# Kernel tuning notes

Measured on AMD Instinct MI355X. Metric: run time of the kernel, lower is better.

Reference implementation:

```python
import jax, jax.numpy as jnp
import numpy as np

H = 256
EPS = 1e-5
RBF_GAMMA = 10.0
RBF_CENTERS = jnp.asarray(np.arange(0.0, np.pi, 0.1), dtype=jnp.float32)  # 32 centers


def layer_norm(x, g, b):
    m = x.mean(-1, keepdims=True)
    v = ((x - m) ** 2).mean(-1, keepdims=True)
    return (x - m) * jax.lax.rsqrt(v + EPS) * g + b


def gin(src, dst, n_nodes, node_feat, edge_feat, w1, b1, w2, b2):
    # message = h_src + h_edge ; sum-aggregate at dst ; 2-layer MLP
    msg = node_feat[src] + edge_feat                                  # [E, H]
    agg = jax.ops.segment_sum(msg, dst, num_segments=n_nodes)        # [N, H]
    return jax.nn.relu(agg @ w1 + b1) @ w2 + b2


def graph_normal(gid, n_graphs, x):
    # divide each node feature by sqrt(#nodes in its graph)
    cnt = jax.ops.segment_sum(jnp.ones((x.shape[0],), x.dtype), gid, num_segments=n_graphs)
    return x * jax.lax.rsqrt(jnp.maximum(cnt, 1.0))[gid][:, None]


def geognn_block(src, dst, gid, n_graphs, node_hidden, edge_feat, w1, b1, w2, b2, ln_g, ln_b):
    out = gin(src, dst, node_hidden.shape[0], node_hidden, edge_feat, w1, b1, w2, b2)
    out = layer_norm(out, ln_g, ln_b)
    out = graph_normal(gid, n_graphs, out)
    # activation=False, dropout is identity in eval mode
    return out + node_hidden


def setup_inputs() -> dict:
    key = jax.random.key(0)
    ks = jax.random.split(key, 24)
    N, E, A, G = 65536, 131072, 262144, 2048
    nC = RBF_CENTERS.shape[0]
    s = 1.0 / np.sqrt(H)
    inp = {
        "node_hidden": jax.random.normal(ks[0], (N, H), jnp.float32),
        "edge_hidden": jax.random.normal(ks[1], (E, H), jnp.float32),
        "bond_angle": jax.random.uniform(ks[2], (A,), jnp.float32) * np.float32(np.pi),
        "ab_src": jax.random.randint(ks[3], (N * 2,), 0, N).astype(jnp.int64)[:E],
        "ab_dst": jax.random.randint(ks[4], (E,), 0, N).astype(jnp.int64),
        "ba_src": jax.random.randint(ks[5], (A,), 0, E).astype(jnp.int64),
        "ba_dst": jax.random.randint(ks[6], (A,), 0, E).astype(jnp.int64),
        "node_gid": jnp.sort(jax.random.randint(ks[7], (N,), 0, G)).astype(jnp.int64),
        "bond_gid": jnp.sort(jax.random.randint(ks[8], (E,), 0, G)).astype(jnp.int64),
        "num_graphs": G,
        # bond-angle RBF linear
        "rbf_w": jax.random.normal(ks[9], (nC, H), jnp.float32) / np.sqrt(nC),
        "rbf_b": jnp.zeros((H,), jnp.float32),
        # bond_angle_gnn (GIN MLP + LayerNorm)
        "ba_w1": jax.random.normal(ks[10], (H, 2 * H), jnp.float32) * s,
        "ba_b1": jnp.zeros((2 * H,), jnp.float32),
        "ba_w2": jax.random.normal(ks[11], (2 * H, H), jnp.float32) * s,
        "ba_b2": jnp.zeros((H,), jnp.float32),
        "ba_ln_g": jnp.ones((H,), jnp.float32),
        "ba_ln_b": jnp.zeros((H,), jnp.float32),
        # atom_bond_gnn
        "ab_w1": jax.random.normal(ks[12], (H, 2 * H), jnp.float32) * s,
        "ab_b1": jnp.zeros((2 * H,), jnp.float32),
        "ab_w2": jax.random.normal(ks[13], (2 * H, H), jnp.float32) * s,
        "ab_b2": jnp.zeros((H,), jnp.float32),
        "ab_ln_g": jnp.ones((H,), jnp.float32),
        "ab_ln_b": jnp.zeros((H,), jnp.float32),
    }
    return inp


def reference(node_hidden, edge_hidden, bond_angle, ab_src, ab_dst, ba_src, ba_dst,
              node_gid, bond_gid, num_graphs, rbf_w, rbf_b,
              ba_w1, ba_b1, ba_w2, ba_b2, ba_ln_g, ba_ln_b,
              ab_w1, ab_b1, ab_w2, ab_b2, ab_ln_g, ab_ln_b):
    # RBF encode bond angles -> angle edge features [A, H]
    rbf = jnp.exp(-RBF_GAMMA * (bond_angle[:, None] - RBF_CENTERS[None, :]) ** 2)
    angle_hidden = rbf @ rbf_w + rbf_b
    # bond-angle GNN updates bond features (nodes of bond_angle graph)
    edge_out = geognn_block(ba_src, ba_dst, bond_gid, num_graphs,
                            edge_hidden, angle_hidden,
                            ba_w1, ba_b1, ba_w2, ba_b2, ba_ln_g, ba_ln_b)
    # atom-bond GNN updates atom features using updated bond features as edge feats
    node_out = geognn_block(ab_src, ab_dst, node_gid, num_graphs,
                            node_hidden, edge_out,
                            ab_w1, ab_b1, ab_w2, ab_b2, ab_ln_g, ab_ln_b)
    # average pooling over atoms per graph
    cnt = jax.ops.segment_sum(jnp.ones((node_out.shape[0],), node_out.dtype), node_gid,
                              num_segments=num_graphs)
    graph_repr = jax.ops.segment_sum(node_out, node_gid, num_segments=num_graphs) / jnp.maximum(cnt, 1.0)[:, None]
    return node_out, edge_out, graph_repr
```

## Files before the change

### kernel.cpp

```cpp
#include <hip/hip_runtime.h>

#define HDIM 256
#define LNEPS 1e-5f

typedef float f32x4 __attribute__((ext_vector_type(4)));
typedef short bf16x8 __attribute__((ext_vector_type(8)));

static __device__ __forceinline__ unsigned short f2b(float f) {
  union { float f; unsigned u; } v; v.f = f;
  return (unsigned short)((v.u + 0x7fffu + ((v.u >> 16) & 1u)) >> 16);
}
static __device__ __forceinline__ unsigned pk2(float lo, float hi) {
  return (unsigned)f2b(lo) | ((unsigned)f2b(hi) << 16);
}

__global__ void pack_all_kernel(const float* __restrict__ w1a, const float* __restrict__ w2a,
                                const float* __restrict__ w1b, const float* __restrict__ w2b,
                                unsigned short* __restrict__ o1a, unsigned short* __restrict__ o2a,
                                unsigned short* __restrict__ o1b, unsigned short* __restrict__ o2b) {
  int sel = blockIdx.x >> 9;
  int o = (blockIdx.x & 511) * 256 + threadIdx.x;
  if (sel == 0 || sel == 2) {
    const float* in = (sel == 0) ? w1a : w1b;
    unsigned short* out = (sel == 0) ? o1a : o1b;
    int ke = o & 7, n1l = (o >> 3) & 127, lg = (o >> 10) & 3, sl = o >> 12;
    int h = sl >> 3, kk = sl & 7;
    int k = kk * 32 + lg * 8 + ke, n1 = h * 128 + n1l;
    out[o] = f2b(in[k * 512 + n1]);
  } else {
    const float* in = (sel == 1) ? w2a : w2b;
    unsigned short* out = (sel == 1) ? o2a : o2b;
    int ke = o & 7, n2l = (o >> 3) & 127, lg = (o >> 10) & 3, sl = o >> 12;
    int h = sl >> 3, r = sl & 7, h2 = r >> 2, kk2 = r & 3;
    int k2 = h * 128 + kk2 * 32 + lg * 8 + ke, n2 = h2 * 128 + n2l;
    out[o] = f2b(in[k2 * 256 + n2]);
  }
}

__global__ void prep_kernel(const int* __restrict__ node_gid, const int* __restrict__ bond_gid,
                            const int* __restrict__ ab_dst, const int* __restrict__ ba_dst,
                            int* cnt_node, int* cnt_bond, int* deg_n, int* deg_e,
                            int N, int E, int A) {
  int i = blockIdx.x * 256 + threadIdx.x;
  if (i < N) atomicAdd(&cnt_node[node_gid[i]], 1);
  if (i < E) {
    atomicAdd(&cnt_bond[bond_gid[i]], 1);
    atomicAdd(&deg_n[ab_dst[i]], 1);
  }
  if (i < A) atomicAdd(&deg_e[ba_dst[i]], 1);
}

__global__ void scan1_both_kernel(const int* __restrict__ degE, const int* __restrict__ degN,
                                  int* __restrict__ offE, int* __restrict__ offN,
                                  int* __restrict__ bsum, int E, int N, int nbE) {
  int b = blockIdx.x;
  const int* deg; int* excl; int* bs; int n; int bb;
  if (b < nbE) { deg = degE; excl = offE; bs = bsum; n = E; bb = b; }
  else { deg = degN; excl = offN; bs = bsum + 512; n = N; bb = b - nbE; }
  int t = threadIdx.x;
  int i = bb * 256 + t;
  int v = (i < n) ? deg[i] : 0;
  int lane = t & 63, w = t >> 6;
  int s = v;
#pragma unroll
  for (int d = 1; d < 64; d <<= 1) {
    int u = __shfl_up(s, d);
    if (lane >= d) s += u;
  }
  __shared__ int wsum[4];
  if (lane == 63) wsum[w] = s;
  __syncthreads();
  int base = 0;
  for (int ww = 0; ww < w; ++ww) base += wsum[ww];
  if (i < n) excl[i] = base + s - v;
  if (t == 255) bs[bb] = base + s;
}

__global__ void scan2_both_kernel(int* __restrict__ bsum, int nbE, int nbN) {
  int* bs = bsum + blockIdx.x * 512;
  int nb = (blockIdx.x == 0) ? nbE : nbN;
  int t = threadIdx.x;
  int v = (t < nb) ? bs[t] : 0;
  int lane = t & 63, w = t >> 6;
  int s = v;
#pragma unroll
  for (int d = 1; d < 64; d <<= 1) {
    int u = __shfl_up(s, d);
    if (lane >= d) s += u;
  }
  __shared__ int wsum[16];
  if (lane == 63) wsum[w] = s;
  __syncthreads();
  int base = 0;
  for (int ww = 0; ww < w; ++ww) base += wsum[ww];
  if (t < nb) bs[t] = base + s - v;
}

__global__ void scan3f_kernel(int* __restrict__ offE, int* __restrict__ offN,
                              const int* __restrict__ bsum,
                              const int* __restrict__ cnt_node, const int* __restrict__ cnt_bond,
                              float* fac_node, float* fac_bond, float* recip_node,
                              int E, int N, int G, int nbE, int nbN) {
  int b = blockIdx.x;
  if (b < nbE) {
    int i = b * 256 + threadIdx.x;
    if (i < E) offE[i] += bsum[b];
  } else if (b < nbE + nbN) {
    int bb = b - nbE;
    int i = bb * 256 + threadIdx.x;
    if (i < N) offN[i] += bsum[512 + bb];
  } else {
    int g = (b - nbE - nbN) * 256 + threadIdx.x;
    if (g < G) {
      float cn = fmaxf((float)cnt_node[g], 1.f);
      float cb = fmaxf((float)cnt_bond[g], 1.f);
      fac_node[g] = rsqrtf(cn);
      fac_bond[g] = rsqrtf(cb);
      recip_node[g] = 1.f / cn;
    }
  }
}

__global__ void fill_both_kernel(const int* __restrict__ ba_dst, const int* __restrict__ ab_dst,
                                 const int* __restrict__ offE, const int* __restrict__ offN,
                                 int* __restrict__ curE, int* __restrict__ curN,
                                 int* __restrict__ csrE, int* __restrict__ csrN,
                                 int A, int E, int nbA) {
  int b = blockIdx.x;
  if (b < nbA) {
    int i = b * 256 + threadIdx.x;
    if (i < A) {
      int d = ba_dst[i];
      int p = atomicAdd(&curE[d], 1);
      csrE[offE[d] + p] = i;
    }
  } else {
    int i = (b - nbA) * 256 + threadIdx.x;
    if (i < E) {
      int d = ab_dst[i];
      int p = atomicAdd(&curN[d], 1);
      csrN[offN[d] + p] = i;
    }
  }
}

__global__ __launch_bounds__(256) void angle_gather_kernel(
    const float* __restrict__ bond_angle, const int* __restrict__ ba_src,
    const float* __restrict__ edge_hidden,
    const int* __restrict__ off, const int* __restrict__ deg, const int* __restrict__ csr,
    const float* __restrict__ rbf_w, const float* __restrict__ rbf_b,
    float* __restrict__ agg_e, int E) {
  __shared__ float rbfw_s[32 * 256];
  int t = threadIdx.x;
  int w = t >> 6, lane = t & 63;
#pragma unroll
  for (int i = 0; i < 8; ++i)
    *(f32x4*)&rbfw_s[(t + i * 256) * 4] = *(const f32x4*)&rbf_w[(t + i * 256) * 4];
  __syncthreads();
  int c4 = lane * 4;
  f32x4 bv = *(const f32x4*)&rbf_b[c4];
  float cc = 0.1f * (float)(lane & 31);
  for (int rr = 0; rr < 2; ++rr) {
    int d = blockIdx.x * 8 + w * 2 + rr;
    if (d >= E) break;
    int start = off[d], cnt = deg[d];
    f32x4 acc = (f32x4)0.f;
    float rbfs = 0.f;
    for (int base = 0; base < cnt; base += 64) {
      int n = cnt - base; if (n > 64) n = 64;
      float av = 0.f;
      int s = 0;
      if (lane < n) {
        int a = csr[start + base + lane];
        av = bond_angle[a];
        s = ba_src[a];
      }
#pragma unroll 4
      for (int i = 0; i < n; ++i) {
        float avi = __shfl(av, i);
        int si = __shfl(s, i);
        if (lane < 32) {
          float dd = avi - cc;
          rbfs += __expf(-10.f * dd * dd);
        }
        acc += *(const f32x4*)&edge_hidden[(size_t)si * HDIM + c4];
      }
    }
#pragma unroll 8
    for (int k = 0; k < 32; ++k) {
      float rv = __shfl(rbfs, k);
      f32x4 wv = *(const f32x4*)&rbfw_s[k * 256 + c4];
      acc[0] += rv * wv[0]; acc[1] += rv * wv[1];
      acc[2] += rv * wv[2]; acc[3] += rv * wv[3];
    }
    float fc = (float)cnt;
    acc[0] += fc * bv[0]; acc[1] += fc * bv[1];
    acc[2] += fc * bv[2]; acc[3] += fc * bv[3];
    *(f32x4*)&agg_e[(size_t)d * HDIM + c4] = acc;
  }
}

__global__ __launch_bounds__(256) void node_gather_kernel(
    const float* __restrict__ node_hidden, const float* __restrict__ edge_out,
    const int* __restrict__ ab_src,
    const int* __restrict__ off, const int* __restrict__ deg, const int* __restrict__ csr,
    float* __restrict__ agg_n, int N) {
  int w = threadIdx.x >> 6, lane = threadIdx.x & 63;
  int d = blockIdx.x * 4 + w;
  if (d >= N) return;
  int c4 = lane * 4;
  int start = off[d], cnt = deg[d];
  f32x4 acc = (f32x4)0.f;
  for (int base = 0; base < cnt; base += 64) {
    int n = cnt - base; if (n > 64) n = 64;
    int e = 0, s = 0;
    if (lane < n) {
      e = csr[start + base + lane];
      s = ab_src[e];
    }
#pragma unroll 4
    for (int i = 0; i < n; ++i) {
      int ei = __shfl(e, i);
      int si = __shfl(s, i);
      f32x4 a = *(const f32x4*)&edge_out[(size_t)ei * HDIM + c4];
      f32x4 b = *(const f32x4*)&node_hidden[(size_t)si * HDIM + c4];
      acc += a;
      acc += b;
    }
  }
  *(f32x4*)&agg_n[(size_t)d * HDIM + c4] = acc;
}

template <int POOL>
__global__ __launch_bounds__(256, 4) void mlp_kernel(
    const float* agg_in, float* out_rows,
    const float* __restrict__ residual, const int* __restrict__ gid,
    const float* __restrict__ gfactor,
    const unsigned short* __restrict__ w1p, const float* __restrict__ b1,
    const unsigned short* __restrict__ w2p, const float* __restrict__ b2,
    const float* __restrict__ ln_g, const float* __restrict__ ln_b,
    float* pool_out, int M) {
  __shared__ __align__(16) char smem[40960];
  char* Xb = smem;
  char* Hb = smem + 16384;
  char* Wb = smem + 24576;
  char* OutsB = smem;
  float* psA = (float*)(smem + 32768);
  float* psB = (float*)(smem + 33280);
  float* fstat = (float*)(smem + 33792);
  float* gfs = (float*)(smem + 34048);
  int* gid_s = (int*)(smem + 34176);

  int t = threadIdx.x;
  int row0 = blockIdx.x * 32;
  int w = t >> 6, lane = t & 63;
  int l15 = lane & 15, lg = lane >> 4;

  auto slab_ptr = [&](int ss) -> const uint4* {
    int hh = ss >> 4, r = ss & 15;
    const unsigned short* p = (r < 8) ? (w1p + (size_t)(hh * 8 + r) * 4096)
                                      : (w2p + (size_t)(hh * 8 + (r - 8)) * 4096);
    return (const uint4*)p;
  };

  uint4 rA0, rA1, rB0, rB1;

  {
    const uint4* g0 = slab_ptr(0);
    uint4 s0a = g0[t], s0b = g0[t + 256];
    const uint4* g1 = slab_ptr(1);
    rA0 = g1[t]; rA1 = g1[t + 256];
    int row = t >> 3;
    int c0 = (t & 7) * 32;
    int gr = row0 + row; if (gr >= M) gr = M - 1;
    const float* src = agg_in + (size_t)gr * HDIM + c0;
#pragma unroll
    for (int i = 0; i < 4; ++i) {
      f32x4 a = *(const f32x4*)(src + i * 8);
      f32x4 b = *(const f32x4*)(src + i * 8 + 4);
      int byte = (row * 512 + (c0 + i * 8) * 2) ^ ((row & 7) << 4);
      *(uint4*)(Xb + byte) =
          make_uint4(pk2(a[0], a[1]), pk2(a[2], a[3]), pk2(b[0], b[1]), pk2(b[2], b[3]));
    }
    *(uint4*)(Wb + t * 16) = s0a;
    *(uint4*)(Wb + (t + 256) * 16) = s0b;
  }
  __syncthreads();

  f32x4 acc2[2][4];
#pragma unroll
  for (int mt = 0; mt < 2; ++mt)
#pragma unroll
    for (int nf = 0; nf < 4; ++nf) acc2[mt][nf] = (f32x4)0.f;

  int s = 0;
  for (int h = 0; h < 4; ++h) {
    f32x4 acc1[2][2];
#pragma unroll
    for (int tt = 0; tt < 2; ++tt)
#pragma unroll
      for (int mt = 0; mt < 2; ++mt) acc1[tt][mt] = (f32x4)0.f;

    for (int kk = 0; kk < 8; ++kk) {
      if (s + 2 < 64) { const uint4* g = slab_ptr(s + 2); rB0 = g[t]; rB1 = g[t + 256]; }
      const char* buf = Wb + (s & 1) * 8192;
      bf16x8 xfr[2], afr[2];
#pragma unroll
      for (int mt = 0; mt < 2; ++mt) {
        int m = mt * 16 + l15;
        int byte = (m * 512 + kk * 64 + lg * 16) ^ ((m & 7) << 4);
        xfr[mt] = *(const bf16x8*)(Xb + byte);
      }
#pragma unroll
      for (int tt = 0; tt < 2; ++tt)
        afr[tt] = *(const bf16x8*)(buf + lg * 2048 + (w * 32 + tt * 16 + l15) * 16);
#pragma unroll
      for (int tt = 0; tt < 2; ++tt)
#pragma unroll
        for (int mt = 0; mt < 2; ++mt)
          acc1[tt][mt] = __builtin_amdgcn_mfma_f32_16x16x32_bf16(afr[tt], xfr[mt], acc1[tt][mt], 0, 0, 0);

      if (kk == 7) {
#pragma unroll
        for (int tt = 0; tt < 2; ++tt) {
          f32x4 b1v = *(const f32x4*)&b1[h * 128 + w * 32 + tt * 16 + lg * 4];
#pragma unroll
          for (int mt = 0; mt < 2; ++mt) {
            f32x4 v = acc1[tt][mt] + b1v;
            v[0] = fmaxf(v[0], 0.f); v[1] = fmaxf(v[1], 0.f);
            v[2] = fmaxf(v[2], 0.f); v[3] = fmaxf(v[3], 0.f);
            int m = mt * 16 + l15;
            int n1l = w * 32 + tt * 16 + lg * 4;
            int byte = (m * 256 + n1l * 2) ^ ((m & 7) << 4);
            *(uint2*)(Hb + byte) = make_uint2(pk2(v[0], v[1]), pk2(v[2], v[3]));
          }
        }
      }
      if (s + 1 < 64) {
        char* nb = Wb + ((s + 1) & 1) * 8192;
        *(uint4*)(nb + t * 16) = rA0;
        *(uint4*)(nb + (t + 256) * 16) = rA1;
      }
      __syncthreads();
      rA0 = rB0; rA1 = rB1;
      ++s;
    }

#pragma unroll
    for (int h2 = 0; h2 < 2; ++h2) {
#pragma unroll
      for (int kk2 = 0; kk2 < 4; ++kk2) {
        if (s + 2 < 64) { const uint4* g = slab_ptr(s + 2); rB0 = g[t]; rB1 = g[t + 256]; }
        const char* buf = Wb + (s & 1) * 8192;
        bf16x8 hfr[2], wfr[2];
#pragma unroll
        for (int mt = 0; mt < 2; ++mt) {
          int m = mt * 16 + l15;
          int byte = (m * 256 + kk2 * 64 + lg * 16) ^ ((m & 7) << 4);
          hfr[mt] = *(const bf16x8*)(Hb + byte);
        }
#pragma unroll
        for (int nf = 0; nf < 2; ++nf)
          wfr[nf] = *(const bf16x8*)(buf + lg * 2048 + (w * 32 + nf * 16 + l15) * 16);
#pragma unroll
        for (int mt = 0; mt < 2; ++mt)
#pragma unroll
          for (int nf = 0; nf < 2; ++nf)
            acc2[mt][h2 * 2 + nf] =
                __builtin_amdgcn_mfma_f32_16x16x32_bf16(hfr[mt], wfr[nf], acc2[mt][h2 * 2 + nf], 0, 0, 0);
        if (s + 1 < 64) {
          char* nb = Wb + ((s + 1) & 1) * 8192;
          *(uint4*)(nb + t * 16) = rA0;
          *(uint4*)(nb + (t + 256) * 16) = rA1;
        }
        __syncthreads();
        rA0 = rB0; rA1 = rB1;
        ++s;
      }
    }
  }

  {
    float rs[2][4], rss[2][4];
#pragma unroll
    for (int mt = 0; mt < 2; ++mt)
#pragma unroll
      for (int jr = 0; jr < 4; ++jr) { rs[mt][jr] = 0.f; rss[mt][jr] = 0.f; }
#pragma unroll
    for (int nfi = 0; nfi < 4; ++nfi) {
      int col = (nfi >> 1) * 128 + w * 32 + (nfi & 1) * 16 + l15;
      float b2v = b2[col];
#pragma unroll
      for (int mt = 0; mt < 2; ++mt)
#pragma unroll
        for (int jr = 0; jr < 4; ++jr) {
          float v = acc2[mt][nfi][jr] + b2v;
          int row = mt * 16 + lg * 4 + jr;
          *(float*)(OutsB + (((row * 256 + col) * 4) ^ ((row & 7) << 4))) = v;
          rs[mt][jr] += v;
          rss[mt][jr] += v * v;
        }
    }
#pragma unroll
    for (int mt = 0; mt < 2; ++mt)
#pragma unroll
      for (int jr = 0; jr < 4; ++jr) {
        float sv = rs[mt][jr], ssv = rss[mt][jr];
        sv += __shfl_xor(sv, 1); ssv += __shfl_xor(ssv, 1);
        sv += __shfl_xor(sv, 2); ssv += __shfl_xor(ssv, 2);
        sv += __shfl_xor(sv, 4); ssv += __shfl_xor(ssv, 4);
        sv += __shfl_xor(sv, 8); ssv += __shfl_xor(ssv, 8);
        if (l15 == 0) {
          int r = mt * 16 + lg * 4 + jr;
          psA[r * 4 + w] = sv;
          psB[r * 4 + w] = ssv;
        }
      }
    if (t < 32) {
      int r = row0 + t;
      int g = (r < M) ? gid[r] : 0;
      gid_s[t] = g;
      gfs[t] = gfactor[g];
    }
  }
  __syncthreads();
  if (t < 32) {
    float sv = psA[t * 4] + psA[t * 4 + 1] + psA[t * 4 + 2] + psA[t * 4 + 3];
    float ssv = psB[t * 4] + psB[t * 4 + 1] + psB[t * 4 + 2] + psB[t * 4 + 3];
    float mean = sv * (1.f / 256.f);
    float var = ssv * (1.f / 256.f) - mean * mean;
    fstat[t * 2] = mean;
    fstat[t * 2 + 1] = rsqrtf(var + LNEPS);
  }
  __syncthreads();

  {
    float g_t = ln_g[t], bb_t = ln_b[t];
    float psum = 0.f;
    int curg = -1;
#pragma unroll 4
    for (int p = 0; p < 32; ++p) {
      int gr = row0 + p;
      if (gr < M) {
        float v = *(const float*)(OutsB + (((p * 256 + t) * 4) ^ ((p & 7) << 4)));
        v = (v - fstat[p * 2]) * fstat[p * 2 + 1] * g_t + bb_t;
        v *= gfs[p];
        v += residual[(size_t)gr * HDIM + t];
        out_rows[(size_t)gr * HDIM + t] = v;
        if (POOL) {
          int g = gid_s[p];
          if (g != curg) {
            if (curg >= 0) atomicAdd(&pool_out[(size_t)curg * HDIM + t], psum);
            psum = 0.f;
            curg = g;
          }
          psum += v;
        }
      }
    }
    if (POOL && curg >= 0) atomicAdd(&pool_out[(size_t)curg * HDIM + t], psum);
  }
}

__global__ void pooldiv_kernel(float* out_graph, const float* __restrict__ recip_node) {
  int g = blockIdx.x, t = threadIdx.x;
  out_graph[(size_t)g * HDIM + t] *= recip_node[g];
}

extern "C" void kernel_launch(void* const* d_in, const int* in_sizes, int n_in,
                              void* d_out, int out_size, void* d_ws, size_t ws_size,
                              hipStream_t stream) {
  const float* node_hidden = (const float*)d_in[0];
  const float* edge_hidden = (const float*)d_in[1];
  const float* bond_angle = (const float*)d_in[2];
  const int* ab_src = (const int*)d_in[3];
  const int* ab_dst = (const int*)d_in[4];
  const int* ba_src = (const int*)d_in[5];
  const int* ba_dst = (const int*)d_in[6];
  const int* node_gid = (const int*)d_in[7];
  const int* bond_gid = (const int*)d_in[8];
  const float* rbf_w = (const float*)d_in[10];
  const float* rbf_b = (const float*)d_in[11];
  const float* ba_w1 = (const float*)d_in[12];
  const float* ba_b1 = (const float*)d_in[13];
  const float* ba_w2 = (const float*)d_in[14];
  const float* ba_b2 = (const float*)d_in[15];
  const float* ba_ln_g = (const float*)d_in[16];
  const float* ba_ln_b = (const float*)d_in[17];
  const float* ab_w1 = (const float*)d_in[18];
  const float* ab_b1 = (const float*)d_in[19];
  const float* ab_w2 = (const float*)d_in[20];
  const float* ab_b2 = (const float*)d_in[21];
  const float* ab_ln_g = (const float*)d_in[22];
  const float* ab_ln_b = (const float*)d_in[23];

  int N = in_sizes[0] / HDIM;
  int E = in_sizes[1] / HDIM;
  int A = in_sizes[2];
  int G = out_size / HDIM - N - E;

  float* out_node = (float*)d_out;
  float* out_edge = out_node + (size_t)N * HDIM;
  float* out_graph = out_edge + (size_t)E * HDIM;

  char* ws = (char*)d_ws;
  int* cnt_node = (int*)ws;
  int* cnt_bond = cnt_node + G;
  int* deg_e = cnt_bond + G;
  int* cur_e = deg_e + E;
  int* deg_n = cur_e + E;
  int* cur_n = deg_n + N;
  size_t zero_bytes = (size_t)(2 * G + 2 * E + 2 * N) * 4;
  float* fac_node = (float*)(cur_n + N);
  float* fac_bond = fac_node + G;
  float* recip_node = fac_bond + G;
  int* off_e = (int*)(recip_node + G);
  int* csr_e = off_e + E;
  int* off_n = csr_e + A;
  int* csr_n = off_n + N;
  int* bsum = csr_n + E;
  size_t off = ((size_t)((char*)(bsum + 1024) - ws) + 255) & ~(size_t)255;
  unsigned short* w1p_ba = (unsigned short*)(ws + off); off += (size_t)512 * 256 * 2;
  unsigned short* w2p_ba = (unsigned short*)(ws + off); off += (size_t)256 * 512 * 2;
  unsigned short* w1p_ab = (unsigned short*)(ws + off); off += (size_t)512 * 256 * 2;
  unsigned short* w2p_ab = (unsigned short*)(ws + off); off += (size_t)256 * 512 * 2;

  hipMemsetAsync(d_ws, 0, zero_bytes, stream);
  hipMemsetAsync(out_graph, 0, (size_t)G * HDIM * 4, stream);

  pack_all_kernel<<<2048, 256, 0, stream>>>(ba_w1, ba_w2, ab_w1, ab_w2,
                                            w1p_ba, w2p_ba, w1p_ab, w2p_ab);

  prep_kernel<<<(A + 255) / 256, 256, 0, stream>>>(node_gid, bond_gid, ab_dst, ba_dst,
                                                   cnt_node, cnt_bond, deg_n, deg_e, N, E, A);

  int nbE = (E + 255) / 256;
  int nbN = (N + 255) / 256;
  int nbA = (A + 255) / 256;
  int nbG = (G + 255) / 256;
  scan1_both_kernel<<<nbE + nbN, 256, 0, stream>>>(deg_e, deg_n, off_e, off_n, bsum, E, N, nbE);
  scan2_both_kernel<<<2, 1024, 0, stream>>>(bsum, nbE, nbN);
  scan3f_kernel<<<nbE + nbN + nbG, 256, 0, stream>>>(off_e, off_n, bsum, cnt_node, cnt_bond,
                                                     fac_node, fac_bond, recip_node,
                                                     E, N, G, nbE, nbN);
  fill_both_kernel<<<nbA + nbE, 256, 0, stream>>>(ba_dst, ab_dst, off_e, off_n,
                                                  cur_e, cur_n, csr_e, csr_n, A, E, nbA);

  angle_gather_kernel<<<(E + 7) / 8, 256, 0, stream>>>(bond_angle, ba_src, edge_hidden,
                                                       off_e, deg_e, csr_e, rbf_w, rbf_b,
                                                       out_edge, E);
  mlp_kernel<0><<<(E + 31) / 32, 256, 0, stream>>>(out_edge, out_edge, edge_hidden, bond_gid,
                                                   fac_bond, w1p_ba, ba_b1, w2p_ba, ba_b2,
                                                   ba_ln_g, ba_ln_b, nullptr, E);

  node_gather_kernel<<<(N + 3) / 4, 256, 0, stream>>>(node_hidden, out_edge, ab_src,
                                                      off_n, deg_n, csr_n, out_node, N);
  mlp_kernel<1><<<(N + 31) / 32, 256, 0, stream>>>(out_node, out_node, node_hidden, node_gid,
                                                   fac_node, w1p_ab, ab_b1, w2p_ab, ab_b2,
                                                   ab_ln_g, ab_ln_b, out_graph, N);

  pooldiv_kernel<<<G, 256, 0, stream>>>(out_graph, recip_node);
}
```

Before: 593.8 us.

## Stream MLP weight slabs via per-wave direct-to-LDS loads, drop per-slab barriers

Weight packing is reordered so each wave owns a contiguous 2KB slice of every slab. The MLP kernel then streams those slices straight into a per-wave double-buffered LDS ring using global_load_lds, instead of staging through registers with a block-wide __syncthreads per slab. Block barriers are now needed only around the hidden-activation handoff, which is meant to cut synchronisation and register-staging overhead in the weight pipeline. Each step waits on vmcnt(0), so the prefetch distance is only one slab, and load latency may be exposed.

```diff
diff --git a/kernel.cpp b/kernel.cpp
--- a/kernel.cpp
+++ b/kernel.cpp
@@ -12,6 +12,11 @@
 }
 static __device__ __forceinline__ unsigned pk2(float lo, float hi) {
   return (unsigned)f2b(lo) | ((unsigned)f2b(hi) << 16);
+}
+
+static __device__ __forceinline__ void gload_lds16(const void* g, void* l) {
+  __builtin_amdgcn_global_load_lds((const __attribute__((address_space(1))) unsigned int*)g,
+                                   (__attribute__((address_space(3))) unsigned int*)l, 16, 0, 0);
 }
 
 __global__ void pack_all_kernel(const float* __restrict__ w1a, const float* __restrict__ w2a,
@@ -20,19 +25,21 @@
                                 unsigned short* __restrict__ o1b, unsigned short* __restrict__ o2b) {
   int sel = blockIdx.x >> 9;
   int o = (blockIdx.x & 511) * 256 + threadIdx.x;
+  int ke = o & 7, lane = (o >> 3) & 63, tt = (o >> 9) & 1, w = (o >> 10) & 3, sl = o >> 12;
+  int l15 = lane & 15, lg = lane >> 4;
   if (sel == 0 || sel == 2) {
     const float* in = (sel == 0) ? w1a : w1b;
     unsigned short* out = (sel == 0) ? o1a : o1b;
-    int ke = o & 7, n1l = (o >> 3) & 127, lg = (o >> 10) & 3, sl = o >> 12;
     int h = sl >> 3, kk = sl & 7;
-    int k = kk * 32 + lg * 8 + ke, n1 = h * 128 + n1l;
+    int n1 = h * 128 + w * 32 + tt * 16 + l15;
+    int k = kk * 32 + lg * 8 + ke;
     out[o] = f2b(in[k * 512 + n1]);
   } else {
     const float* in = (sel == 1) ? w2a : w2b;
     unsigned short* out = (sel == 1) ? o2a : o2b;
-    int ke = o & 7, n2l = (o >> 3) & 127, lg = (o >> 10) & 3, sl = o >> 12;
-    int h = sl >> 3, r = sl & 7, h2 = r >> 2, kk2 = r & 3;
-    int k2 = h * 128 + kk2 * 32 + lg * 8 + ke, n2 = h2 * 128 + n2l;
+    int h = sl >> 3, q = sl & 7, h2 = q >> 2, kk2 = q & 3;
+    int n2 = h2 * 128 + w * 32 + tt * 16 + l15;
+    int k2 = h * 128 + kk2 * 32 + lg * 8 + ke;
     out[o] = f2b(in[k2 * 256 + n2]);
   }
 }
@@ -243,7 +250,7 @@
   __shared__ __align__(16) char smem[40960];
   char* Xb = smem;
   char* Hb = smem + 16384;
-  char* Wb = smem + 24576;
+  char* Wr = smem + 24576;
   char* OutsB = smem;
   float* psA = (float*)(smem + 32768);
   float* psB = (float*)(smem + 33280);
@@ -256,20 +263,19 @@
   int w = t >> 6, lane = t & 63;
   int l15 = lane & 15, lg = lane >> 4;
 
-  auto slab_ptr = [&](int ss) -> const uint4* {
+  char* ring = Wr + w * 4096;
+  auto issue_slab = [&](int ss) {
     int hh = ss >> 4, r = ss & 15;
     const unsigned short* p = (r < 8) ? (w1p + (size_t)(hh * 8 + r) * 4096)
                                       : (w2p + (size_t)(hh * 8 + (r - 8)) * 4096);
-    return (const uint4*)p;
+    const char* g = (const char*)p + w * 2048 + lane * 16;
+    char* dst = ring + (ss & 1) * 2048;
+    gload_lds16(g, dst);
+    gload_lds16(g + 1024, dst + 1024);
   };
 
-  uint4 rA0, rA1, rB0, rB1;
-
+  issue_slab(0);
   {
-    const uint4* g0 = slab_ptr(0);
-    uint4 s0a = g0[t], s0b = g0[t + 256];
-    const uint4* g1 = slab_ptr(1);
-    rA0 = g1[t]; rA1 = g1[t + 256];
     int row = t >> 3;
     int c0 = (t & 7) * 32;
     int gr = row0 + row; if (gr >= M) gr = M - 1;
@@ -282,8 +288,6 @@
       *(uint4*)(Xb + byte) =
           make_uint4(pk2(a[0], a[1]), pk2(a[2], a[3]), pk2(b[0], b[1]), pk2(b[2], b[3]));
     }
-    *(uint4*)(Wb + t * 16) = s0a;
-    *(uint4*)(Wb + (t + 256) * 16) = s0b;
   }
   __syncthreads();
 
@@ -293,7 +297,6 @@
 #pragma unroll
     for (int nf = 0; nf < 4; ++nf) acc2[mt][nf] = (f32x4)0.f;
 
-  int s = 0;
   for (int h = 0; h < 4; ++h) {
     f32x4 acc1[2][2];
 #pragma unroll
@@ -301,83 +304,67 @@
 #pragma unroll
       for (int mt = 0; mt < 2; ++mt) acc1[tt][mt] = (f32x4)0.f;
 
+#pragma unroll
     for (int kk = 0; kk < 8; ++kk) {
-      if (s + 2 < 64) { const uint4* g = slab_ptr(s + 2); rB0 = g[t]; rB1 = g[t + 256]; }
-      const char* buf = Wb + (s & 1) * 8192;
-      bf16x8 xfr[2], afr[2];
+      asm volatile("s_waitcnt vmcnt(0)" ::: "memory");
+      const char* wbuf = ring + (kk & 1) * 2048;
+      bf16x8 afr0 = *(const bf16x8*)(wbuf + lane * 16);
+      bf16x8 afr1 = *(const bf16x8*)(wbuf + 1024 + lane * 16);
+      bf16x8 xfr0, xfr1;
+      {
+        int byte0 = (l15 * 512 + kk * 64 + lg * 16) ^ ((l15 & 7) << 4);
+        xfr0 = *(const bf16x8*)(Xb + byte0);
+        int m = 16 + l15;
+        int byte1 = (m * 512 + kk * 64 + lg * 16) ^ ((m & 7) << 4);
+        xfr1 = *(const bf16x8*)(Xb + byte1);
+      }
+      __builtin_amdgcn_sched_barrier(0);
+      issue_slab(h * 16 + kk + 1);
+      acc1[0][0] = __builtin_amdgcn_mfma_f32_16x16x32_bf16(afr0, xfr0, acc1[0][0], 0, 0, 0);
+      acc1[0][1] = __builtin_amdgcn_mfma_f32_16x16x32_bf16(afr0, xfr1, acc1[0][1], 0, 0, 0);
+      acc1[1][0] = __builtin_amdgcn_mfma_f32_16x16x32_bf16(afr1, xfr0, acc1[1][0], 0, 0, 0);
+      acc1[1][1] = __builtin_amdgcn_mfma_f32_16x16x32_bf16(afr1, xfr1, acc1[1][1], 0, 0, 0);
+    }
+
+#pragma unroll
+    for (int tt = 0; tt < 2; ++tt) {
+      f32x4 b1v = *(const f32x4*)&b1[h * 128 + w * 32 + tt * 16 + lg * 4];
 #pragma unroll
       for (int mt = 0; mt < 2; ++mt) {
+        f32x4 v = acc1[tt][mt] + b1v;
+        v[0] = fmaxf(v[0], 0.f); v[1] = fmaxf(v[1], 0.f);
+        v[2] = fmaxf(v[2], 0.f); v[3] = fmaxf(v[3], 0.f);
         int m = mt * 16 + l15;
-        int byte = (m * 512 + kk * 64 + lg * 16) ^ ((m & 7) << 4);
-        xfr[mt] = *(const bf16x8*)(Xb + byte);
-      }
-#pragma unroll
-      for (int tt = 0; tt < 2; ++tt)
-        afr[tt] = *(const bf16x8*)(buf + lg * 2048 + (w * 32 + tt * 16 + l15) * 16);
-#pragma unroll
-      for (int tt = 0; tt < 2; ++tt)
-#pragma unroll
-        for (int mt = 0; mt < 2; ++mt)
-          acc1[tt][mt] = __builtin_amdgcn_mfma_f32_16x16x32_bf16(afr[tt], xfr[mt], acc1[tt][mt], 0, 0, 0);
-
-      if (kk == 7) {
-#pragma unroll
-        for (int tt = 0; tt < 2; ++tt) {
-          f32x4 b1v = *(const f32x4*)&b1[h * 128 + w * 32 + tt * 16 + lg * 4];
-#pragma unroll
-          for (int mt = 0; mt < 2; ++mt) {
-            f32x4 v = acc1[tt][mt] + b1v;
-            v[0] = fmaxf(v[0], 0.f); v[1] = fmaxf(v[1], 0.f);
-            v[2] = fmaxf(v[2], 0.f); v[3] = fmaxf(v[3], 0.f);
-            int m = mt * 16 + l15;
-            int n1l = w * 32 + tt * 16 + lg * 4;
-            int byte = (m * 256 + n1l * 2) ^ ((m & 7) << 4);
-            *(uint2*)(Hb + byte) = make_uint2(pk2(v[0], v[1]), pk2(v[2], v[3]));
-          }
-        }
-      }
-      if (s + 1 < 64) {
-        char* nb = Wb + ((s + 1) & 1) * 8192;
-        *(uint4*)(nb + t * 16) = rA0;
-        *(uint4*)(nb + (t + 256) * 16) = rA1;
-      }
-      __syncthreads();
-      rA0 = rB0; rA1 = rB1;
-      ++s;
-    }
-
-#pragma unroll
-    for (int h2 = 0; h2 < 2; ++h2) {
-#pragma unroll
-      for (int kk2 = 0; kk2 < 4; ++kk2) {
-        if (s + 2 < 64) { const uint4* g = slab_ptr(s + 2); rB0 = g[t]; rB1 = g[t + 256]; }
-        const char* buf = Wb + (s & 1) * 8192;
-        bf16x8 hfr[2], wfr[2];
-#pragma unroll
-        for (int mt = 0; mt < 2; ++mt) {
-          int m = mt * 16 + l15;
-          int byte = (m * 256 + kk2 * 64 + lg * 16) ^ ((m & 7) << 4);
-          hfr[mt] = *(const bf16x8*)(Hb + byte);
-        }
-#pragma unroll
-        for (int nf = 0; nf < 2; ++nf)
-          wfr[nf] = *(const bf16x8*)(buf + lg * 2048 + (w * 32 + nf * 16 + l15) * 16);
-#pragma unroll
-        for (int mt = 0; mt < 2; ++mt)
-#pragma unroll
-          for (int nf = 0; nf < 2; ++nf)
-            acc2[mt][h2 * 2 + nf] =
-                __builtin_amdgcn_mfma_f32_16x16x32_bf16(hfr[mt], wfr[nf], acc2[mt][h2 * 2 + nf], 0, 0, 0);
-        if (s + 1 < 64) {
-          char* nb = Wb + ((s + 1) & 1) * 8192;
-          *(uint4*)(nb + t * 16) = rA0;
-          *(uint4*)(nb + (t + 256) * 16) = rA1;
-        }
-        __syncthreads();
-        rA0 = rB0; rA1 = rB1;
-        ++s;
-      }
-    }
+        int n1l = w * 32 + tt * 16 + lg * 4;
+        int byte = (m * 256 + n1l * 2) ^ ((m & 7) << 4);
+        *(uint2*)(Hb + byte) = make_uint2(pk2(v[0], v[1]), pk2(v[2], v[3]));
+      }
+    }
+    __syncthreads();
+
+#pragma unroll
+    for (int q = 0; q < 8; ++q) {
+      asm volatile("s_waitcnt vmcnt(0)" ::: "memory");
+      const char* wbuf = ring + (q & 1) * 2048;
+      bf16x8 wfr0 = *(const bf16x8*)(wbuf + lane * 16);
+      bf16x8 wfr1 = *(const bf16x8*)(wbuf + 1024 + lane * 16);
+      int kk2 = q & 3, h2 = q >> 2;
+      bf16x8 hfr0, hfr1;
+      {
+        int byte0 = (l15 * 256 + kk2 * 64 + lg * 16) ^ ((l15 & 7) << 4);
+        hfr0 = *(const bf16x8*)(Hb + byte0);
+        int m = 16 + l15;
+        int byte1 = (m * 256 + kk2 * 64 + lg * 16) ^ ((m & 7) << 4);
+        hfr1 = *(const bf16x8*)(Hb + byte1);
+      }
+      __builtin_amdgcn_sched_barrier(0);
+      if (h < 3 || q < 7) issue_slab(h * 16 + 9 + q);
+      acc2[0][h2 * 2 + 0] = __builtin_amdgcn_mfma_f32_16x16x32_bf16(hfr0, wfr0, acc2[0][h2 * 2 + 0], 0, 0, 0);
+      acc2[0][h2 * 2 + 1] = __builtin_amdgcn_mfma_f32_16x16x32_bf16(hfr0, wfr1, acc2[0][h2 * 2 + 1], 0, 0, 0);
+      acc2[1][h2 * 2 + 0] = __builtin_amdgcn_mfma_f32_16x16x32_bf16(hfr1, wfr0, acc2[1][h2 * 2 + 0], 0, 0, 0);
+      acc2[1][h2 * 2 + 1] = __builtin_amdgcn_mfma_f32_16x16x32_bf16(hfr1, wfr1, acc2[1][h2 * 2 + 1], 0, 0, 0);
+    }
+    __syncthreads();
   }
 
   {
```

Result: slower. 622.0 us (+4.7%).
